# Kernel tuning notes

Measured on AMD Instinct MI355X. Metric: run time of the kernel, lower is better.

## Reference

```python
import jax, jax.numpy as jnp
import numpy as np

N_NODES, N_EDGES, N_GRAPHS = 30000, 70000, 1024
TOWERS, F_IN, F_OUT, N_LAYERS = 5, 75, 15, 4
DEG_HIST = np.array([0.0, 100.0, 400.0, 300.0, 50.0], dtype=np.float32)
AVG_DEG_LOG = float((np.log(np.arange(len(DEG_HIST)) + 1.0) * DEG_HIST).sum() / DEG_HIST.sum())


def setup_inputs():
    key = jax.random.key(0)
    ks = jax.random.split(key, 16)
    g = lambda k, shp, fan: jax.random.normal(k, shp, jnp.float32) * (1.0 / np.sqrt(fan))
    return dict(
        x=jax.random.randint(ks[0], (N_NODES,), 0, 21),
        edge_index=jax.random.randint(ks[1], (2, N_EDGES), 0, N_NODES),
        edge_attr=jax.random.randint(ks[2], (N_EDGES,), 0, 4),
        batch=jnp.sort(jax.random.randint(ks[3], (N_NODES,), 0, N_GRAPHS)),
        node_emb=g(ks[4], (21, 75), 75),
        edge_emb=g(ks[5], (4, 50), 50),
        enc_w=g(ks[6], (N_LAYERS, 50, 75), 50),
        enc_b=jnp.zeros((N_LAYERS, 75), jnp.float32),
        pre_w=g(ks[7], (N_LAYERS, TOWERS, 3 * F_IN, F_IN), 3 * F_IN),
        pre_b=jnp.zeros((N_LAYERS, TOWERS, F_IN), jnp.float32),
        post_w=g(ks[8], (N_LAYERS, TOWERS, 13 * F_IN, F_OUT), 13 * F_IN),
        post_b=jnp.zeros((N_LAYERS, TOWERS, F_OUT), jnp.float32),
        lin_w=g(ks[9], (N_LAYERS, 75, 75), 75),
        lin_b=jnp.zeros((N_LAYERS, 75), jnp.float32),
        bn_g=jnp.ones((N_LAYERS, 75), jnp.float32),
        bn_b=jnp.zeros((N_LAYERS, 75), jnp.float32),
        mlp_w1=g(ks[10], (75, 50), 75), mlp_b1=jnp.zeros((50,), jnp.float32),
        mlp_w2=g(ks[11], (50, 25), 50), mlp_b2=jnp.zeros((25,), jnp.float32),
        mlp_w3=g(ks[12], (25, 1), 25), mlp_b3=jnp.zeros((1,), jnp.float32),
    )


def _pna_layer(h, src, dst, e_enc, pw, pb, qw, qb, lw, lb):
    n = h.shape[0]
    # message: cat[x_i, x_j, edge_enc] shared across towers, per-tower pre-NN
    msg = jnp.concatenate([h[dst], h[src], e_enc], axis=-1)            # [E, 3*F_in]
    m = jnp.einsum('ef,tfo->eto', msg, pw) + pb                        # [E, T, F_in]
    deg = jax.ops.segment_sum(jnp.ones((m.shape[0],), m.dtype), dst, n)
    has = (deg > 0)[:, None, None]
    cnt = jnp.maximum(deg, 1.0)[:, None, None]                         # clamp(1)
    mean = jax.ops.segment_sum(m, dst, n) / cnt
    mean_sq = jax.ops.segment_sum(m * m, dst, n) / cnt
    std = jnp.sqrt(jax.nn.relu(mean_sq - mean * mean) + 1e-5)
    mn = jnp.where(has, jax.ops.segment_min(m, dst, n), 0.0)
    mx = jnp.where(has, jax.ops.segment_max(m, dst, n), 0.0)
    agg = jnp.concatenate([mean, mn, mx, std], axis=-1)                # [N, T, 4*F_in]
    amp = jnp.log(cnt + 1.0) / AVG_DEG_LOG                             # amplification scaler
    scaled = jnp.concatenate([agg, agg * amp, agg / amp], axis=-1)     # [N, T, 12*F_in]
    post_in = jnp.concatenate(
        [jnp.broadcast_to(h[:, None, :], (n, TOWERS, F_IN)), scaled], axis=-1)  # [N, T, 13*F_in]
    out = jnp.einsum('ntf,tfo->nto', post_in, qw) + qb                 # [N, T, F_out]
    return out.reshape(n, TOWERS * F_OUT) @ lw + lb                    # [N, 75]


def _bn_relu(h, g, b):
    mu = h.mean(axis=0)
    var = h.var(axis=0)
    return jax.nn.relu((h - mu) * jax.lax.rsqrt(var + 1e-5) * g + b)


def reference(x, edge_index, edge_attr, batch, node_emb, edge_emb, enc_w, enc_b,
              pre_w, pre_b, post_w, post_b, lin_w, lin_b, bn_g, bn_b,
              mlp_w1, mlp_b1, mlp_w2, mlp_b2, mlp_w3, mlp_b3):
    h = node_emb[x]                      # [N, 75]
    e = edge_emb[edge_attr]              # [E, 50]
    src, dst = edge_index[0], edge_index[1]
    for l in range(N_LAYERS):
        e_enc = e @ enc_w[l] + enc_b[l]  # [E, 75]
        h = _bn_relu(_pna_layer(h, src, dst, e_enc, pre_w[l], pre_b[l],
                                post_w[l], post_b[l], lin_w[l], lin_b[l]),
                     bn_g[l], bn_b[l])
    hg = jax.ops.segment_sum(h, batch, N_GRAPHS)   # global_add_pool -> [G, 75]
    z = jax.nn.relu(hg @ mlp_w1 + mlp_b1)
    z = jax.nn.relu(z @ mlp_w2 + mlp_b2)
    return z @ mlp_w3 + mlp_b3
```

## Files before the change

### kernel.cpp

```cpp
#include <hip/hip_runtime.h>
#include <hip/hip_bf16.h>
#include <float.h>
#include <math.h>

#define NN 30000
#define NE 70000
#define NG 1024
#define NT 5
#define FI 75
#define NL 4

#define AMP_DENOM 1.1824939264481302f

#define ABW 832
#define AGW 1600
#define HBW 96
#define ZW 76

typedef __attribute__((ext_vector_type(8))) short bf16x8;
typedef __attribute__((ext_vector_type(4))) float f32x4;

__device__ __forceinline__ float bf2f(unsigned short u) {
    return __uint_as_float(((unsigned int)u) << 16);
}
__device__ __forceinline__ unsigned short f2bf(float f) {
    __hip_bfloat16 h = __float2bfloat16(f);
    return *reinterpret_cast<unsigned short*>(&h);
}

__global__ __launch_bounds__(256) void k_deg(const int* __restrict__ dst, int* __restrict__ deg) {
    int e = blockIdx.x * 256 + threadIdx.x;
    if (e < NE) atomicAdd(&deg[dst[e]], 1);
}

__global__ __launch_bounds__(1024) void k_scan(const int* __restrict__ deg, int* __restrict__ rowptr) {
    __shared__ int wsum[16];
    __shared__ int s_carry;
    int tid = threadIdx.x;
    int lane = tid & 63, wv = tid >> 6;
    if (tid == 0) s_carry = 0;
    __syncthreads();
    for (int base = 0; base < NN; base += 1024) {
        int i = base + tid;
        int v = (i < NN) ? deg[i] : 0;
        int x = v;
        #pragma unroll
        for (int off = 1; off < 64; off <<= 1) {
            int t = __shfl_up(x, off);
            if (lane >= off) x += t;
        }
        if (lane == 63) wsum[wv] = x;
        __syncthreads();
        if (tid < 16) {
            int y = wsum[tid];
            #pragma unroll
            for (int off = 1; off < 16; off <<= 1) {
                int t = __shfl_up(y, off);
                if (tid >= off) y += t;
            }
            wsum[tid] = y;
        }
        __syncthreads();
        int wbase = ((wv > 0) ? wsum[wv - 1] : 0) + s_carry;
        if (i < NN) rowptr[i] = wbase + x - v;
        int tot = wsum[15];
        __syncthreads();
        if (tid == 0) s_carry += tot;
    }
    __syncthreads();
    if (tid == 0) rowptr[NN] = s_carry;
}

__global__ __launch_bounds__(256) void k_scatter(const int* __restrict__ src, const int* __restrict__ dst,
                                                 const int* __restrict__ attr, const int* __restrict__ rowptr,
                                                 int* __restrict__ fill, int* __restrict__ csr) {
    int e = blockIdx.x * 256 + threadIdx.x;
    if (e < NE) {
        int d = dst[e];
        int pos = rowptr[d] + atomicAdd(&fill[d], 1);
        csr[pos] = src[e] | (attr[e] << 20);
    }
}

__global__ __launch_bounds__(256) void k_amp(const int* __restrict__ rowptr,
                                             float* __restrict__ amp, float* __restrict__ inv) {
    int n = blockIdx.x * 256 + threadIdx.x;
    if (n < NN) {
        int dg = rowptr[n + 1] - rowptr[n];
        float cnt = fmaxf((float)dg, 1.0f);
        float a = logf(cnt + 1.0f) * (1.0f / AMP_DENOM);
        amp[n] = a;
        inv[n] = 1.0f / a;
    }
}

__global__ __launch_bounds__(256) void k_h0(const int* __restrict__ x, const float* __restrict__ emb,
                                            unsigned short* __restrict__ hb) {
    int idx = blockIdx.x * 256 + threadIdx.x;
    if (idx < NN * HBW) {
        int n = idx / HBW, f = idx % HBW;
        hb[idx] = (f < FI) ? f2bf(emb[x[n] * FI + f]) : (unsigned short)0;
    }
}

__global__ __launch_bounds__(256) void k_wprep5(const float* __restrict__ post_w,
                                                unsigned short* __restrict__ Wp5) {
    int idx = blockIdx.x * 256 + threadIdx.x;
    if (idx >= NL * NT * 3 * 10 * 512) return;
    int e = idx & 7;
    int lane = (idx >> 3) & 63;
    int ks = (idx >> 9) % 10;
    int s = (idx / 5120) % 3;
    int t = (idx / 15360) % NT;
    int l = idx / 76800;
    int lr = lane & 15, lq = lane >> 4;
    int kk = ks * 32 + lq * 8 + e;
    float val = 0.0f;
    if (kk < 304 && lr < 15) {
        int stat = kk / 76, of = kk - stat * 76;
        if (of < 75)
            val = post_w[((size_t)(l * NT + t) * 975 + 75 + s * 300 + stat * 75 + of) * 15 + lr];
    }
    Wp5[idx] = f2bf(val);
}

__global__ __launch_bounds__(256) void k_wprep2f(const float* __restrict__ pre_w,
                                                 const float* __restrict__ post_w,
                                                 unsigned short* __restrict__ Wp2f) {
    int idx = blockIdx.x * 256 + threadIdx.x;
    if (idx >= NL * 52 * 3 * 512) return;
    int e = idx & 7;
    int lane = (idx >> 3) & 63;
    int ks = (idx >> 9) % 3;
    int nt = (idx / 1536) % 52;
    int l = idx / (1536 * 52);
    int lr = lane & 15, lq = lane >> 4;
    int j = nt * 16 + lr;
    int k = ks * 32 + lq * 8 + e;
    float val = 0.0f;
    if (k < 75 && j < 825) {
        if (j < 375) {
            int t = j / 75, o = j % 75;
            val = pre_w[((size_t)(l * NT + t) * 225 + k) * FI + o];
        } else if (j < 750) {
            int jm = j - 375;
            int t = jm / 75, o = jm % 75;
            val = pre_w[((size_t)(l * NT + t) * 225 + 75 + k) * FI + o];
        } else {
            int c = j - 750;
            int t = c / 15, o = c % 15;
            val = post_w[((size_t)(l * NT + t) * 975 + k) * 15 + o];
        }
    }
    Wp2f[idx] = f2bf(val);
}

__global__ __launch_bounds__(256) void k_wprep4(const float* __restrict__ lin_w,
                                                unsigned short* __restrict__ linTp) {
    int idx = blockIdx.x * 256 + threadIdx.x;
    if (idx >= NL * 5 * 3 * 512) return;
    int e = idx & 7;
    int lane = (idx >> 3) & 63;
    int ks = (idx >> 9) % 3;
    int nt = (idx / 1536) % 5;
    int l = idx / 7680;
    int lr = lane & 15, lq = lane >> 4;
    int c = nt * 16 + lr;
    int k = ks * 32 + lq * 8 + e;
    float v = 0.0f;
    if (k < 75 && c < 75) v = lin_w[(size_t)l * 5625 + k * 75 + c];
    linTp[idx] = f2bf(v);
}

__global__ __launch_bounds__(384) void k_tbl4(const float* __restrict__ edge_emb, const float* __restrict__ enc_w,
                                              const float* __restrict__ enc_b, const float* __restrict__ pre_w,
                                              const float* __restrict__ pre_b, float* __restrict__ tbl4) {
    __shared__ float e4[4][FI];
    int l = blockIdx.x;
    int tid = threadIdx.x;
    float* tbl = tbl4 + l * 1500;
    if (tid < 300) {
        int a = tid / FI, f = tid % FI;
        float acc = enc_b[l * FI + f];
        for (int k = 0; k < 50; k++)
            acc += edge_emb[a * 50 + k] * enc_w[(l * 50 + k) * FI + f];
        e4[a][f] = acc;
    }
    __syncthreads();
    for (int idx = tid; idx < 4 * 375; idx += 384) {
        int a = idx / 375, c = idx % 375;
        int t = c / FI, o = c % FI;
        const float* wp = pre_w + ((size_t)(l * NT + t) * 225 + 150) * FI + o;
        float acc = pre_b[(l * NT + t) * FI + o];
        for (int f = 0; f < FI; f++)
            acc += e4[a][f] * wp[f * FI];
        tbl[idx] = acc;
    }
}

__global__ __launch_bounds__(256) void k_bnh(const float* __restrict__ z, const float* __restrict__ bnsum,
                                             const float* __restrict__ bng, const float* __restrict__ bnb,
                                             unsigned short* __restrict__ hb) {
    __shared__ float s_sc[75], s_sh[75];
    int tid = threadIdx.x;
    if (tid < 75) {
        float mu = bnsum[tid] * (1.0f / NN);
        float msq = bnsum[76 + tid] * (1.0f / NN);
        float var = msq - mu * mu;
        float sc = rsqrtf(var + 1e-5f) * bng[tid];
        s_sc[tid] = sc;
        s_sh[tid] = bnb[tid] - mu * sc;
    }
    __syncthreads();
    int idx = blockIdx.x * 256 + tid;
    if (idx < NN * HBW) {
        int n = idx / HBW, c = idx % HBW;
        float v = 0.0f;
        if (c < 75) v = fmaxf(z[(size_t)n * ZW + c] * s_sc[c] + s_sh[c], 0.0f);
        hb[idx] = (c < 75) ? f2bf(v) : (unsigned short)0;
    }
}

__global__ __launch_bounds__(256) void k_preab(const unsigned short* __restrict__ hb,
                                               const unsigned short* __restrict__ Wp2f,
                                               int l, __hip_bfloat16* __restrict__ ABH) {
    __shared__ __align__(16) unsigned short sA[128 * 104];
    int tid = threadIdx.x;
    int m0 = blockIdx.x * 128;
    int jt0 = blockIdx.y * 13;

    const uint4* hsrc = (const uint4*)hb;
    for (int c = tid; c < 128 * 12; c += 256) {
        int r = c / 12, q = c % 12;
        int n = m0 + r;
        uint4 v = make_uint4(0, 0, 0, 0);
        if (n < NN) v = hsrc[(size_t)n * 12 + q];
        *(uint4*)&sA[r * 104 + q * 8] = v;
    }
    __syncthreads();

    int w = tid >> 6, lane = tid & 63;
    int mw = w * 32;
    int lr = lane & 15, lq = lane >> 4;

    bf16x8 af[2][3];
    #pragma unroll
    for (int mt = 0; mt < 2; mt++)
        #pragma unroll
        for (int ks = 0; ks < 3; ks++)
            af[mt][ks] = *(const bf16x8*)&sA[(mw + mt * 16 + lr) * 104 + ks * 32 + lq * 8];

    f32x4 acc[13][2];
    #pragma unroll
    for (int nt = 0; nt < 13; nt++)
        #pragma unroll
        for (int mt = 0; mt < 2; mt++)
            acc[nt][mt] = (f32x4){0.0f, 0.0f, 0.0f, 0.0f};

    const unsigned short* wp = Wp2f + ((size_t)l * 52 + jt0) * 3 * 512;
    #pragma unroll
    for (int nt = 0; nt < 13; nt++) {
        #pragma unroll
        for (int ks = 0; ks < 3; ks++) {
            bf16x8 bf = *(const bf16x8*)&wp[(nt * 3 + ks) * 512 + lane * 8];
            acc[nt][0] = __builtin_amdgcn_mfma_f32_16x16x32_bf16(bf, af[0][ks], acc[nt][0], 0, 0, 0);
            acc[nt][1] = __builtin_amdgcn_mfma_f32_16x16x32_bf16(bf, af[1][ks], acc[nt][1], 0, 0, 0);
        }
    }

    unsigned short* abo = (unsigned short*)ABH;
    int j0 = jt0 * 16;
    #pragma unroll
    for (int mt = 0; mt < 2; mt++) {
        int n = m0 + mw + mt * 16 + lr;
        if (n < NN) {
            #pragma unroll
            for (int nt = 0; nt < 13; nt++) {
                int c0 = j0 + nt * 16 + lq * 4;
                ushort4 us;
                us.x = f2bf(acc[nt][mt][0]);
                us.y = f2bf(acc[nt][mt][1]);
                us.z = f2bf(acc[nt][mt][2]);
                us.w = f2bf(acc[nt][mt][3]);
                *(ushort4*)&abo[(size_t)n * ABW + c0] = us;
            }
        }
    }
}

__global__ __launch_bounds__(256) void k_gather(const __hip_bfloat16* __restrict__ ABH,
                                                const float* __restrict__ tbl,
                                                const int* __restrict__ rowptr, const int* __restrict__ csr,
                                                unsigned short* __restrict__ AGG) {
    __shared__ float s_tbl[1500];
    int tid = threadIdx.x;
    for (int i = tid; i < 1500; i += 256) s_tbl[i] = tbl[i];
    __syncthreads();

    int w = tid >> 6, l = tid & 63;
    int n = blockIdx.x * 4 + w;
    int base = rowptr[n];
    int dg = rowptr[n + 1] - base;

    float sum[6], ss[6], mn[6], mx[6];
    #pragma unroll
    for (int j = 0; j < 6; j++) { sum[j] = 0.f; ss[j] = 0.f; mn[j] = FLT_MAX; mx[j] = -FLT_MAX; }

    const unsigned short* abu = (const unsigned short*)ABH;
    int k = 0;
    for (; k + 1 < dg; k += 2) {
        int pk0 = csr[base + k], pk1 = csr[base + k + 1];
        const unsigned short* bp0 = abu + (size_t)(pk0 & 0xFFFFF) * ABW + 375;
        const unsigned short* bp1 = abu + (size_t)(pk1 & 0xFFFFF) * ABW + 375;
        const float* tp0 = s_tbl + (pk0 >> 20) * 375;
        const float* tp1 = s_tbl + (pk1 >> 20) * 375;
        #pragma unroll
        for (int j = 0; j < 6; j++) {
            int f = l + 64 * j;
            if (f < 375) {
                float v0 = bf2f(bp0[f]) + tp0[f];
                float v1 = bf2f(bp1[f]) + tp1[f];
                sum[j] += v0 + v1;
                ss[j] += v0 * v0 + v1 * v1;
                mn[j] = fminf(mn[j], fminf(v0, v1));
                mx[j] = fmaxf(mx[j], fmaxf(v0, v1));
            }
        }
    }
    if (k < dg) {
        int pk0 = csr[base + k];
        const unsigned short* bp0 = abu + (size_t)(pk0 & 0xFFFFF) * ABW + 375;
        const float* tp0 = s_tbl + (pk0 >> 20) * 375;
        #pragma unroll
        for (int j = 0; j < 6; j++) {
            int f = l + 64 * j;
            if (f < 375) {
                float v0 = bf2f(bp0[f]) + tp0[f];
                sum[j] += v0; ss[j] += v0 * v0;
                mn[j] = fminf(mn[j], v0); mx[j] = fmaxf(mx[j], v0);
            }
        }
    }

    unsigned short* out = AGG + (size_t)n * AGW;
    if (dg > 0) {
        float rc = 1.0f / (float)dg;
        const unsigned short* ap = abu + (size_t)n * ABW;
        #pragma unroll
        for (int j = 0; j < 6; j++) {
            int f = l + 64 * j;
            if (f < 375) {
                int t = f / 75, of = f - t * 75;
                int o = t * 320 + of;
                float Af = bf2f(ap[f]);
                float mean = sum[j] * rc;
                float var = ss[j] * rc - mean * mean;
                out[o]       = f2bf(Af + mean);
                out[o + 76]  = f2bf(Af + mn[j]);
                out[o + 152] = f2bf(Af + mx[j]);
                out[o + 228] = f2bf(sqrtf(fmaxf(var, 0.0f) + 1e-5f));
            }
        }
    } else {
        unsigned short zz = 0;
        unsigned short sd = f2bf(0.0031622776601683794f);
        #pragma unroll
        for (int j = 0; j < 6; j++) {
            int f = l + 64 * j;
            if (f < 375) {
                int t = f / 75, of = f - t * 75;
                int o = t * 320 + of;
                out[o] = zz; out[o + 76] = zz; out[o + 152] = zz; out[o + 228] = sd;
            }
        }
    }
    for (int i = l; i < 80; i += 64) out[(i >> 4) * 320 + 304 + (i & 15)] = 0;
    if (l < 20) out[(l >> 2) * 320 + (l & 3) * 76 + 75] = 0;
}

__global__ __launch_bounds__(256) void k_post(const __hip_bfloat16* __restrict__ ABH,
                                              const unsigned short* __restrict__ AGG,
                                              const unsigned short* __restrict__ Wp5,
                                              const unsigned short* __restrict__ linTp,
                                              const float* __restrict__ amp_a, const float* __restrict__ inv_a,
                                              const float* __restrict__ post_b, const float* __restrict__ lin_b,
                                              int l, float* __restrict__ z, float* __restrict__ bnsum) {
    __shared__ __align__(16) unsigned short s_y[64 * 104];
    __shared__ float s_bn[152];

    int tid = threadIdx.x;
    int n0 = blockIdx.x * 64;
    int w = tid >> 6, lane = tid & 63;
    int lr = lane & 15, lq = lane >> 4;

    if (tid < 152) s_bn[tid] = 0.0f;
    for (int i = tid; i < 64 * 29; i += 256) {
        int r = i / 29, c = 75 + i % 29;
        s_y[r * 104 + c] = 0;
    }

    const unsigned short* abu = (const unsigned short*)ABH;
    int mynode = n0 + w * 16 + lr;
    int mclamp = (mynode < NN) ? mynode : (NN - 1);
    float amp = amp_a[mclamp], inv = inv_a[mclamp];

    for (int t = 0; t < NT; t++) {
        const unsigned short* wp = Wp5 + (size_t)(l * NT + t) * 3 * 10 * 512;
        const unsigned short* ap = AGG + (size_t)mclamp * AGW + t * 320;

        f32x4 ac0 = {0, 0, 0, 0}, ac1 = {0, 0, 0, 0}, ac2 = {0, 0, 0, 0};
        #pragma unroll
        for (int ks = 0; ks < 10; ks++) {
            bf16x8 a = *(const bf16x8*)&ap[ks * 32 + lq * 8];
            bf16x8 b0 = *(const bf16x8*)&wp[(0 * 10 + ks) * 512 + lane * 8];
            bf16x8 b1 = *(const bf16x8*)&wp[(1 * 10 + ks) * 512 + lane * 8];
            bf16x8 b2 = *(const bf16x8*)&wp[(2 * 10 + ks) * 512 + lane * 8];
            ac0 = __builtin_amdgcn_mfma_f32_16x16x32_bf16(b0, a, ac0, 0, 0, 0);
            ac1 = __builtin_amdgcn_mfma_f32_16x16x32_bf16(b1, a, ac1, 0, 0, 0);
            ac2 = __builtin_amdgcn_mfma_f32_16x16x32_bf16(b2, a, ac2, 0, 0, 0);
        }
        #pragma unroll
        for (int r = 0; r < 4; r++) {
            int f = lq * 4 + r;
            if (f < 15) {
                float qb = post_b[(l * NT + t) * 15 + f];
                float ht = bf2f(abu[(size_t)mclamp * ABW + 750 + t * 15 + f]);
                float y = ac0[r] + amp * ac1[r] + inv * ac2[r] + ht + qb;
                s_y[(w * 16 + lr) * 104 + t * 15 + f] = f2bf(y);
            }
        }
    }
    __syncthreads();

    const unsigned short* lp = linTp + (size_t)l * 5 * 3 * 512;
    bf16x8 ya[3];
    #pragma unroll
    for (int ks = 0; ks < 3; ks++)
        ya[ks] = *(const bf16x8*)&s_y[(w * 16 + lr) * 104 + ks * 32 + lq * 8];

    #pragma unroll
    for (int nt = 0; nt < 5; nt++) {
        f32x4 a2 = {0, 0, 0, 0};
        #pragma unroll
        for (int ks = 0; ks < 3; ks++) {
            bf16x8 bb = *(const bf16x8*)&lp[(nt * 3 + ks) * 512 + lane * 8];
            a2 = __builtin_amdgcn_mfma_f32_16x16x32_bf16(bb, ya[ks], a2, 0, 0, 0);
        }
        int c0 = nt * 16 + lq * 4;
        float v[4], vm[4], vm2[4];
        #pragma unroll
        for (int r = 0; r < 4; r++) {
            int c = c0 + r;
            v[r] = (c < 75) ? (a2[r] + lin_b[l * 75 + c]) : 0.0f;
            bool ok = (c < 75) && (mynode < NN);
            vm[r] = ok ? v[r] : 0.0f;
            vm2[r] = ok ? v[r] * v[r] : 0.0f;
        }
        if (mynode < NN) {
            if (c0 + 3 < 75) {
                float4 st = make_float4(v[0], v[1], v[2], v[3]);
                *(float4*)&z[(size_t)mynode * ZW + c0] = st;
            } else {
                #pragma unroll
                for (int r = 0; r < 4; r++)
                    if (c0 + r < 75) z[(size_t)mynode * ZW + c0 + r] = v[r];
            }
        }
        #pragma unroll
        for (int r = 0; r < 4; r++) {
            #pragma unroll
            for (int off = 1; off < 16; off <<= 1) {
                vm[r] += __shfl_xor(vm[r], off);
                vm2[r] += __shfl_xor(vm2[r], off);
            }
        }
        if (lr == 0) {
            #pragma unroll
            for (int r = 0; r < 4; r++) {
                int c = c0 + r;
                if (c < 75) {
                    atomicAdd(&s_bn[c], vm[r]);
                    atomicAdd(&s_bn[76 + c], vm2[r]);
                }
            }
        }
    }
    __syncthreads();
    if (tid < 75) {
        atomicAdd(&bnsum[tid], s_bn[tid]);
        atomicAdd(&bnsum[76 + tid], s_bn[76 + tid]);
    }
}

__global__ __launch_bounds__(256) void k_pool(const float* __restrict__ z, const float* __restrict__ bnsum3,
                                              const float* __restrict__ bng, const float* __restrict__ bnb,
                                              const int* __restrict__ batch, float* __restrict__ hg) {
    __shared__ float s_sc[75], s_sh[75];
    int tid = threadIdx.x;
    if (tid < 75) {
        float mu = bnsum3[tid] * (1.0f / NN);
        float msq = bnsum3[76 + tid] * (1.0f / NN);
        float var = msq - mu * mu;
        float sc = rsqrtf(var + 1e-5f) * bng[tid];
        s_sc[tid] = sc;
        s_sh[tid] = bnb[tid] - mu * sc;
    }
    __syncthreads();
    int idx = blockIdx.x * 256 + tid;
    if (idx < NN * 75) {
        int n = idx / 75, f = idx % 75;
        float v = fmaxf(z[(size_t)n * ZW + f] * s_sc[f] + s_sh[f], 0.0f);
        atomicAdd(&hg[batch[n] * 75 + f], v);
    }
}

__global__ __launch_bounds__(64) void k_mlp(const float* __restrict__ hg,
                                            const float* __restrict__ w1, const float* __restrict__ b1,
                                            const float* __restrict__ w2, const float* __restrict__ b2,
                                            const float* __restrict__ w3, const float* __restrict__ b3,
                                            float* __restrict__ out) {
    __shared__ float zin[75], z1[50], z2[25];
    int g = blockIdx.x, tid = threadIdx.x;
    for (int k = tid; k < 75; k += 64) zin[k] = hg[g * 75 + k];
    __syncthreads();
    if (tid < 50) {
        float acc = b1[tid];
        for (int k = 0; k < 75; k++) acc += zin[k] * w1[k * 50 + tid];
        z1[tid] = fmaxf(acc, 0.0f);
    }
    __syncthreads();
    if (tid < 25) {
        float acc = b2[tid];
        for (int k = 0; k < 50; k++) acc += z1[k] * w2[k * 25 + tid];
        z2[tid] = fmaxf(acc, 0.0f);
    }
    __syncthreads();
    if (tid == 0) {
        float acc = b3[0];
        for (int k = 0; k < 25; k++) acc += z2[k] * w3[k];
        out[g] = acc;
    }
}

extern "C" void kernel_launch(void* const* d_in, const int* in_sizes, int n_in,
                              void* d_out, int out_size, void* d_ws, size_t ws_size,
                              hipStream_t stream) {
    const int* x        = (const int*)d_in[0];
    const int* ei       = (const int*)d_in[1];
    const int* eattr    = (const int*)d_in[2];
    const int* batch    = (const int*)d_in[3];
    const float* node_emb = (const float*)d_in[4];
    const float* edge_emb = (const float*)d_in[5];
    const float* enc_w  = (const float*)d_in[6];
    const float* enc_b  = (const float*)d_in[7];
    const float* pre_w  = (const float*)d_in[8];
    const float* pre_b  = (const float*)d_in[9];
    const float* post_w = (const float*)d_in[10];
    const float* post_b = (const float*)d_in[11];
    const float* lin_w  = (const float*)d_in[12];
    const float* lin_b  = (const float*)d_in[13];
    const float* bn_g   = (const float*)d_in[14];
    const float* bn_b   = (const float*)d_in[15];
    const float* w1     = (const float*)d_in[16];
    const float* b1     = (const float*)d_in[17];
    const float* w2     = (const float*)d_in[18];
    const float* b2     = (const float*)d_in[19];
    const float* w3     = (const float*)d_in[20];
    const float* b3     = (const float*)d_in[21];

    char* p = (char*)d_ws;
    auto carve = [&](size_t bytes) -> char* {
        char* r = p;
        p += ((bytes + 255) & ~(size_t)255);
        return r;
    };
    __hip_bfloat16* ABH = (__hip_bfloat16*)carve((size_t)NN * ABW * 2);
    unsigned short* AGG = (unsigned short*)carve((size_t)NN * AGW * 2);
    float* z     = (float*)carve((size_t)NN * ZW * 4);
    unsigned short* hb = (unsigned short*)carve((size_t)NN * HBW * 2);
    unsigned short* Wp2f  = (unsigned short*)carve((size_t)NL * 52 * 3 * 512 * 2);
    unsigned short* Wp5   = (unsigned short*)carve((size_t)NL * NT * 3 * 10 * 512 * 2);
    unsigned short* linTp = (unsigned short*)carve((size_t)NL * 5 * 3 * 512 * 2);
    float* tbl4  = (float*)carve((size_t)NL * 1500 * 4);
    int* deg     = (int*)carve(NN * 4);
    int* rowptr  = (int*)carve((NN + 1) * 4);
    int* fill    = (int*)carve(NN * 4);
    int* csr     = (int*)carve(NE * 4);
    float* bnsum = (float*)carve((size_t)NL * 152 * 4);
    float* amp_a = (float*)carve(NN * 4);
    float* inv_a = (float*)carve(NN * 4);
    float* hg    = (float*)carve((size_t)NG * 75 * 4);

    hipMemsetAsync(deg, 0, NN * 4, stream);
    hipMemsetAsync(fill, 0, NN * 4, stream);
    hipMemsetAsync(hg, 0, (size_t)NG * 75 * 4, stream);
    hipMemsetAsync(bnsum, 0, (size_t)NL * 152 * 4, stream);

    k_deg<<<(NE + 255) / 256, 256, 0, stream>>>(ei + NE, deg);
    k_scan<<<1, 1024, 0, stream>>>(deg, rowptr);
    k_scatter<<<(NE + 255) / 256, 256, 0, stream>>>(ei, ei + NE, eattr, rowptr, fill, csr);
    k_amp<<<(NN + 255) / 256, 256, 0, stream>>>(rowptr, amp_a, inv_a);
    k_h0<<<(NN * HBW + 255) / 256, 256, 0, stream>>>(x, node_emb, hb);
    k_wprep5<<<(NL * NT * 3 * 10 * 512 + 255) / 256, 256, 0, stream>>>(post_w, Wp5);
    k_wprep2f<<<(NL * 52 * 3 * 512 + 255) / 256, 256, 0, stream>>>(pre_w, post_w, Wp2f);
    k_wprep4<<<(NL * 5 * 3 * 512 + 255) / 256, 256, 0, stream>>>(lin_w, linTp);
    k_tbl4<<<NL, 384, 0, stream>>>(edge_emb, enc_w, enc_b, pre_w, pre_b, tbl4);

    for (int l = 0; l < NL; l++) {
        if (l > 0)
            k_bnh<<<(NN * HBW + 255) / 256, 256, 0, stream>>>(
                z, bnsum + (l - 1) * 152, bn_g + (l - 1) * 75, bn_b + (l - 1) * 75, hb);
        k_preab<<<dim3((NN + 127) / 128, 4), 256, 0, stream>>>(hb, Wp2f, l, ABH);
        k_gather<<<NN / 4, 256, 0, stream>>>(ABH, tbl4 + l * 1500, rowptr, csr, AGG);
        k_post<<<(NN + 63) / 64, 256, 0, stream>>>(ABH, AGG, Wp5, linTp, amp_a, inv_a,
                                                   post_b, lin_b, l, z, bnsum + l * 152);
    }

    k_pool<<<(NN * 75 + 255) / 256, 256, 0, stream>>>(z, bnsum + 3 * 152, bn_g + 3 * 75, bn_b + 3 * 75,
                                                      batch, hg);
    k_mlp<<<NG, 64, 0, stream>>>(hg, w1, b1, w2, b2, w3, b3, (float*)d_out);
}
```

Before: 590.4 us.

## Fuse neighbor aggregation and post-tower MLP into one kernel via shared memory

Merges the gather/aggregate kernel and the post-NN kernel into a single kernel that handles 16 nodes per block with 5 waves. Aggregated features stay in LDS instead of taking a round trip through a global AGG buffer, and each wave computes one tower and one output tile. This drops the 96 MB-scale AGG write and read plus one launch per layer. In exchange the gather parallelism per block is lower (5 waves share 16 nodes), LDS use per block is larger, and the block count rises, which may hurt occupancy and multiply the BN partial-sum atomics.

After: 787.0 us. +33.3%, slower.

```diff
diff --git a/kernel.cpp b/kernel.cpp
--- a/kernel.cpp
+++ b/kernel.cpp
@@ -13,9 +13,9 @@
 #define AMP_DENOM 1.1824939264481302f
 
 #define ABW 832
-#define AGW 1600
 #define HBW 96
 #define ZW 76
+#define AGS 1608
 
 typedef __attribute__((ext_vector_type(8))) short bf16x8;
 typedef __attribute__((ext_vector_type(4))) float f32x4;
@@ -288,130 +288,127 @@
     }
 }
 
-__global__ __launch_bounds__(256) void k_gather(const __hip_bfloat16* __restrict__ ABH,
-                                                const float* __restrict__ tbl,
-                                                const int* __restrict__ rowptr, const int* __restrict__ csr,
-                                                unsigned short* __restrict__ AGG) {
+__global__ __launch_bounds__(320) void k_gp(const __hip_bfloat16* __restrict__ ABH,
+                                            const float* __restrict__ tbl,
+                                            const int* __restrict__ rowptr, const int* __restrict__ csr,
+                                            const unsigned short* __restrict__ Wp5,
+                                            const unsigned short* __restrict__ linTp,
+                                            const float* __restrict__ amp_a, const float* __restrict__ inv_a,
+                                            const float* __restrict__ post_b, const float* __restrict__ lin_b,
+                                            int l, float* __restrict__ z, float* __restrict__ bnsum) {
+    __shared__ __align__(16) unsigned short s_agg[16 * AGS];
+    __shared__ __align__(16) unsigned short s_y[16 * 104];
     __shared__ float s_tbl[1500];
+    __shared__ float s_bn[152];
+
     int tid = threadIdx.x;
-    for (int i = tid; i < 1500; i += 256) s_tbl[i] = tbl[i];
-    __syncthreads();
-
-    int w = tid >> 6, l = tid & 63;
-    int n = blockIdx.x * 4 + w;
-    int base = rowptr[n];
-    int dg = rowptr[n + 1] - base;
-
-    float sum[6], ss[6], mn[6], mx[6];
-    #pragma unroll
-    for (int j = 0; j < 6; j++) { sum[j] = 0.f; ss[j] = 0.f; mn[j] = FLT_MAX; mx[j] = -FLT_MAX; }
-
-    const unsigned short* abu = (const unsigned short*)ABH;
-    int k = 0;
-    for (; k + 1 < dg; k += 2) {
-        int pk0 = csr[base + k], pk1 = csr[base + k + 1];
-        const unsigned short* bp0 = abu + (size_t)(pk0 & 0xFFFFF) * ABW + 375;
-        const unsigned short* bp1 = abu + (size_t)(pk1 & 0xFFFFF) * ABW + 375;
-        const float* tp0 = s_tbl + (pk0 >> 20) * 375;
-        const float* tp1 = s_tbl + (pk1 >> 20) * 375;
-        #pragma unroll
-        for (int j = 0; j < 6; j++) {
-            int f = l + 64 * j;
-            if (f < 375) {
-                float v0 = bf2f(bp0[f]) + tp0[f];
-                float v1 = bf2f(bp1[f]) + tp1[f];
-                sum[j] += v0 + v1;
-                ss[j] += v0 * v0 + v1 * v1;
-                mn[j] = fminf(mn[j], fminf(v0, v1));
-                mx[j] = fmaxf(mx[j], fmaxf(v0, v1));
-            }
-        }
-    }
-    if (k < dg) {
-        int pk0 = csr[base + k];
-        const unsigned short* bp0 = abu + (size_t)(pk0 & 0xFFFFF) * ABW + 375;
-        const float* tp0 = s_tbl + (pk0 >> 20) * 375;
-        #pragma unroll
-        for (int j = 0; j < 6; j++) {
-            int f = l + 64 * j;
-            if (f < 375) {
-                float v0 = bf2f(bp0[f]) + tp0[f];
-                sum[j] += v0; ss[j] += v0 * v0;
-                mn[j] = fminf(mn[j], v0); mx[j] = fmaxf(mx[j], v0);
-            }
-        }
-    }
-
-    unsigned short* out = AGG + (size_t)n * AGW;
-    if (dg > 0) {
-        float rc = 1.0f / (float)dg;
-        const unsigned short* ap = abu + (size_t)n * ABW;
-        #pragma unroll
-        for (int j = 0; j < 6; j++) {
-            int f = l + 64 * j;
-            if (f < 375) {
-                int t = f / 75, of = f - t * 75;
-                int o = t * 320 + of;
-                float Af = bf2f(ap[f]);
-                float mean = sum[j] * rc;
-                float var = ss[j] * rc - mean * mean;
-                out[o]       = f2bf(Af + mean);
-                out[o + 76]  = f2bf(Af + mn[j]);
-                out[o + 152] = f2bf(Af + mx[j]);
-                out[o + 228] = f2bf(sqrtf(fmaxf(var, 0.0f) + 1e-5f));
-            }
-        }
-    } else {
-        unsigned short zz = 0;
-        unsigned short sd = f2bf(0.0031622776601683794f);
-        #pragma unroll
-        for (int j = 0; j < 6; j++) {
-            int f = l + 64 * j;
-            if (f < 375) {
-                int t = f / 75, of = f - t * 75;
-                int o = t * 320 + of;
-                out[o] = zz; out[o + 76] = zz; out[o + 152] = zz; out[o + 228] = sd;
-            }
-        }
-    }
-    for (int i = l; i < 80; i += 64) out[(i >> 4) * 320 + 304 + (i & 15)] = 0;
-    if (l < 20) out[(l >> 2) * 320 + (l & 3) * 76 + 75] = 0;
-}
-
-__global__ __launch_bounds__(256) void k_post(const __hip_bfloat16* __restrict__ ABH,
-                                              const unsigned short* __restrict__ AGG,
-                                              const unsigned short* __restrict__ Wp5,
-                                              const unsigned short* __restrict__ linTp,
-                                              const float* __restrict__ amp_a, const float* __restrict__ inv_a,
-                                              const float* __restrict__ post_b, const float* __restrict__ lin_b,
-                                              int l, float* __restrict__ z, float* __restrict__ bnsum) {
-    __shared__ __align__(16) unsigned short s_y[64 * 104];
-    __shared__ float s_bn[152];
-
-    int tid = threadIdx.x;
-    int n0 = blockIdx.x * 64;
+    int n0 = blockIdx.x * 16;
     int w = tid >> 6, lane = tid & 63;
     int lr = lane & 15, lq = lane >> 4;
 
+    for (int i = tid; i < 1500; i += 320) s_tbl[i] = tbl[i];
     if (tid < 152) s_bn[tid] = 0.0f;
-    for (int i = tid; i < 64 * 29; i += 256) {
+    for (int i = tid; i < 16 * 100; i += 320) {
+        int node = i / 100, c = i % 100;
+        int pos = (c < 80) ? ((c >> 4) * 320 + 304 + (c & 15))
+                           : (((c - 80) >> 2) * 320 + ((c - 80) & 3) * 76 + 75);
+        s_agg[node * AGS + pos] = 0;
+    }
+    for (int i = tid; i < 16 * 29; i += 320) {
         int r = i / 29, c = 75 + i % 29;
         s_y[r * 104 + c] = 0;
     }
+    __syncthreads();
 
     const unsigned short* abu = (const unsigned short*)ABH;
-    int mynode = n0 + w * 16 + lr;
-    int mclamp = (mynode < NN) ? mynode : (NN - 1);
-    float amp = amp_a[mclamp], inv = inv_a[mclamp];
-
-    for (int t = 0; t < NT; t++) {
+
+    for (int ni = w; ni < 16; ni += 5) {
+        int node = n0 + ni;
+        int base = rowptr[node];
+        int dg = rowptr[node + 1] - base;
+
+        float sum[6], ss[6], mn[6], mx[6];
+        #pragma unroll
+        for (int j = 0; j < 6; j++) { sum[j] = 0.f; ss[j] = 0.f; mn[j] = FLT_MAX; mx[j] = -FLT_MAX; }
+
+        int k = 0;
+        for (; k + 1 < dg; k += 2) {
+            int pk0 = csr[base + k], pk1 = csr[base + k + 1];
+            const unsigned short* bp0 = abu + (size_t)(pk0 & 0xFFFFF) * ABW + 375;
+            const unsigned short* bp1 = abu + (size_t)(pk1 & 0xFFFFF) * ABW + 375;
+            const float* tp0 = s_tbl + (pk0 >> 20) * 375;
+            const float* tp1 = s_tbl + (pk1 >> 20) * 375;
+            #pragma unroll
+            for (int j = 0; j < 6; j++) {
+                int f = lane + 64 * j;
+                if (f < 375) {
+                    float v0 = bf2f(bp0[f]) + tp0[f];
+                    float v1 = bf2f(bp1[f]) + tp1[f];
+                    sum[j] += v0 + v1;
+                    ss[j] += v0 * v0 + v1 * v1;
+                    mn[j] = fminf(mn[j], fminf(v0, v1));
+                    mx[j] = fmaxf(mx[j], fmaxf(v0, v1));
+                }
+            }
+        }
+        if (k < dg) {
+            int pk0 = csr[base + k];
+            const unsigned short* bp0 = abu + (size_t)(pk0 & 0xFFFFF) * ABW + 375;
+            const float* tp0 = s_tbl + (pk0 >> 20) * 375;
+            #pragma unroll
+            for (int j = 0; j < 6; j++) {
+                int f = lane + 64 * j;
+                if (f < 375) {
+                    float v0 = bf2f(bp0[f]) + tp0[f];
+                    sum[j] += v0; ss[j] += v0 * v0;
+                    mn[j] = fminf(mn[j], v0); mx[j] = fmaxf(mx[j], v0);
+                }
+            }
+        }
+
+        unsigned short* out = &s_agg[ni * AGS];
+        if (dg > 0) {
+            float rc = 1.0f / (float)dg;
+            const unsigned short* ap = abu + (size_t)node * ABW;
+            #pragma unroll
+            for (int j = 0; j < 6; j++) {
+                int f = lane + 64 * j;
+                if (f < 375) {
+                    int t = f / 75, of = f - t * 75;
+                    int o = t * 320 + of;
+                    float Af = bf2f(ap[f]);
+                    float mean = sum[j] * rc;
+                    float var = ss[j] * rc - mean * mean;
+                    out[o]       = f2bf(Af + mean);
+                    out[o + 76]  = f2bf(Af + mn[j]);
+                    out[o + 152] = f2bf(Af + mx[j]);
+                    out[o + 228] = f2bf(sqrtf(fmaxf(var, 0.0f) + 1e-5f));
+                }
+            }
+        } else {
+            unsigned short sd = f2bf(0.0031622776601683794f);
+            #pragma unroll
+            for (int j = 0; j < 6; j++) {
+                int f = lane + 64 * j;
+                if (f < 375) {
+                    int t = f / 75, of = f - t * 75;
+                    int o = t * 320 + of;
+                    out[o] = 0; out[o + 76] = 0; out[o + 152] = 0; out[o + 228] = sd;
+                }
+            }
+        }
+    }
+    __syncthreads();
+
+    int mynode = n0 + lr;
+    float amp = amp_a[mynode], inv = inv_a[mynode];
+    {
+        int t = w;
         const unsigned short* wp = Wp5 + (size_t)(l * NT + t) * 3 * 10 * 512;
-        const unsigned short* ap = AGG + (size_t)mclamp * AGW + t * 320;
-
         f32x4 ac0 = {0, 0, 0, 0}, ac1 = {0, 0, 0, 0}, ac2 = {0, 0, 0, 0};
         #pragma unroll
         for (int ks = 0; ks < 10; ks++) {
-            bf16x8 a = *(const bf16x8*)&ap[ks * 32 + lq * 8];
+            bf16x8 a = *(const bf16x8*)&s_agg[lr * AGS + t * 320 + ks * 32 + lq * 8];
             bf16x8 b0 = *(const bf16x8*)&wp[(0 * 10 + ks) * 512 + lane * 8];
             bf16x8 b1 = *(const bf16x8*)&wp[(1 * 10 + ks) * 512 + lane * 8];
             bf16x8 b2 = *(const bf16x8*)&wp[(2 * 10 + ks) * 512 + lane * 8];
@@ -424,22 +421,22 @@
             int f = lq * 4 + r;
             if (f < 15) {
                 float qb = post_b[(l * NT + t) * 15 + f];
-                float ht = bf2f(abu[(size_t)mclamp * ABW + 750 + t * 15 + f]);
+                float ht = bf2f(abu[(size_t)mynode * ABW + 750 + t * 15 + f]);
                 float y = ac0[r] + amp * ac1[r] + inv * ac2[r] + ht + qb;
-                s_y[(w * 16 + lr) * 104 + t * 15 + f] = f2bf(y);
-            }
-        }
-    }
-    __syncthreads();
-
-    const unsigned short* lp = linTp + (size_t)l * 5 * 3 * 512;
-    bf16x8 ya[3];
-    #pragma unroll
-    for (int ks = 0; ks < 3; ks++)
-        ya[ks] = *(const bf16x8*)&s_y[(w * 16 + lr) * 104 + ks * 32 + lq * 8];
-
-    #pragma unroll
-    for (int nt = 0; nt < 5; nt++) {
+                s_y[lr * 104 + t * 15 + f] = f2bf(y);
+            }
+        }
+    }
+    __syncthreads();
+
+    {
+        const unsigned short* lp = linTp + (size_t)l * 5 * 3 * 512;
+        bf16x8 ya[3];
+        #pragma unroll
+        for (int ks = 0; ks < 3; ks++)
+            ya[ks] = *(const bf16x8*)&s_y[lr * 104 + ks * 32 + lq * 8];
+
+        int nt = w;
         f32x4 a2 = {0, 0, 0, 0};
         #pragma unroll
         for (int ks = 0; ks < 3; ks++) {
@@ -452,19 +449,16 @@
         for (int r = 0; r < 4; r++) {
             int c = c0 + r;
             v[r] = (c < 75) ? (a2[r] + lin_b[l * 75 + c]) : 0.0f;
-            bool ok = (c < 75) && (mynode < NN);
-            vm[r] = ok ? v[r] : 0.0f;
-            vm2[r] = ok ? v[r] * v[r] : 0.0f;
-        }
-        if (mynode < NN) {
-            if (c0 + 3 < 75) {
-                float4 st = make_float4(v[0], v[1], v[2], v[3]);
-                *(float4*)&z[(size_t)mynode * ZW + c0] = st;
-            } else {
-                #pragma unroll
-                for (int r = 0; r < 4; r++)
-                    if (c0 + r < 75) z[(size_t)mynode * ZW + c0 + r] = v[r];
-            }
+            vm[r] = (c < 75) ? v[r] : 0.0f;
+            vm2[r] = (c < 75) ? v[r] * v[r] : 0.0f;
+        }
+        if (c0 + 3 < 75) {
+            float4 st = make_float4(v[0], v[1], v[2], v[3]);
+            *(float4*)&z[(size_t)mynode * ZW + c0] = st;
+        } else {
+            #pragma unroll
+            for (int r = 0; r < 4; r++)
+                if (c0 + r < 75) z[(size_t)mynode * ZW + c0 + r] = v[r];
         }
         #pragma unroll
         for (int r = 0; r < 4; r++) {
@@ -575,7 +569,6 @@
         return r;
     };
     __hip_bfloat16* ABH = (__hip_bfloat16*)carve((size_t)NN * ABW * 2);
-    unsigned short* AGG = (unsigned short*)carve((size_t)NN * AGW * 2);
     float* z     = (float*)carve((size_t)NN * ZW * 4);
     unsigned short* hb = (unsigned short*)carve((size_t)NN * HBW * 2);
     unsigned short* Wp2f  = (unsigned short*)carve((size_t)NL * 52 * 3 * 512 * 2);
@@ -611,9 +604,8 @@
             k_bnh<<<(NN * HBW + 255) / 256, 256, 0, stream>>>(
                 z, bnsum + (l - 1) * 152, bn_g + (l - 1) * 75, bn_b + (l - 1) * 75, hb);
         k_preab<<<dim3((NN + 127) / 128, 4), 256, 0, stream>>>(hb, Wp2f, l, ABH);
-        k_gather<<<NN / 4, 256, 0, stream>>>(ABH, tbl4 + l * 1500, rowptr, csr, AGG);
-        k_post<<<(NN + 63) / 64, 256, 0, stream>>>(ABH, AGG, Wp5, linTp, amp_a, inv_a,
-                                                   post_b, lin_b, l, z, bnsum + l * 152);
+        k_gp<<<NN / 16, 320, 0, stream>>>(ABH, tbl4 + l * 1500, rowptr, csr, Wp5, linTp,
+                                          amp_a, inv_a, post_b, lin_b, l, z, bnsum + l * 152);
     }
 
     k_pool<<<(NN * 75 + 255) / 256, 256, 0, stream>>>(z, bnsum + 3 * 152, bn_g + 3 * 75, bn_b + 3 * 75,
```

## Split k_post work across towers per wave and vectorize BN-to-bf16 kernel

Applied to the files above, without the earlier changes.

k_post now processes 16 nodes per block with 5 waves, each wave handling one tower in the post-GEMM and one output tile in the linear GEMM, instead of each wave looping over all 5 towers for its own 16 nodes. This gives 5x more blocks and more parallel waves, meant to cut serial per-wave latency. k_bnh now has each thread produce 8 bf16 outputs from two float4 loads and write them with one 16-byte store, reducing thread count and memory transactions. The bounds checks are dropped because NN is divisible by 16. The cost is that every wave in a k_post block loads the same A rows, and there are more BN atomics per block.

Measured after the change: 727.5 us. 23.2% more time.

```diff
diff --git a/kernel.cpp b/kernel.cpp
--- a/kernel.cpp
+++ b/kernel.cpp
@@ -201,23 +201,46 @@
 __global__ __launch_bounds__(256) void k_bnh(const float* __restrict__ z, const float* __restrict__ bnsum,
                                              const float* __restrict__ bng, const float* __restrict__ bnb,
                                              unsigned short* __restrict__ hb) {
-    __shared__ float s_sc[75], s_sh[75];
+    __shared__ float s_sc[76], s_sh[76];
     int tid = threadIdx.x;
-    if (tid < 75) {
-        float mu = bnsum[tid] * (1.0f / NN);
-        float msq = bnsum[76 + tid] * (1.0f / NN);
-        float var = msq - mu * mu;
-        float sc = rsqrtf(var + 1e-5f) * bng[tid];
-        s_sc[tid] = sc;
-        s_sh[tid] = bnb[tid] - mu * sc;
+    if (tid < 76) {
+        if (tid < 75) {
+            float mu = bnsum[tid] * (1.0f / NN);
+            float msq = bnsum[76 + tid] * (1.0f / NN);
+            float var = msq - mu * mu;
+            float sc = rsqrtf(var + 1e-5f) * bng[tid];
+            s_sc[tid] = sc;
+            s_sh[tid] = bnb[tid] - mu * sc;
+        } else {
+            s_sc[tid] = 0.0f;
+            s_sh[tid] = 0.0f;
+        }
     }
     __syncthreads();
     int idx = blockIdx.x * 256 + tid;
-    if (idx < NN * HBW) {
-        int n = idx / HBW, c = idx % HBW;
-        float v = 0.0f;
-        if (c < 75) v = fmaxf(z[(size_t)n * ZW + c] * s_sc[c] + s_sh[c], 0.0f);
-        hb[idx] = (c < 75) ? f2bf(v) : (unsigned short)0;
+    if (idx < NN * 12) {
+        int n = idx / 12, q = idx % 12;
+        int c0 = q * 8;
+        unsigned short r[8];
+        if (c0 < 72) {
+            float4 a = *(const float4*)&z[(size_t)n * ZW + c0];
+            float4 b = *(const float4*)&z[(size_t)n * ZW + c0 + 4];
+            float vv[8] = {a.x, a.y, a.z, a.w, b.x, b.y, b.z, b.w};
+            #pragma unroll
+            for (int j = 0; j < 8; j++)
+                r[j] = f2bf(fmaxf(vv[j] * s_sc[c0 + j] + s_sh[c0 + j], 0.0f));
+        } else if (c0 == 72) {
+            float4 a = *(const float4*)&z[(size_t)n * ZW + 72];
+            float vv[4] = {a.x, a.y, a.z, a.w};
+            #pragma unroll
+            for (int j = 0; j < 8; j++)
+                r[j] = (j < 3) ? f2bf(fmaxf(vv[j] * s_sc[72 + j] + s_sh[72 + j], 0.0f))
+                               : (unsigned short)0;
+        } else {
+            #pragma unroll
+            for (int j = 0; j < 8; j++) r[j] = 0;
+        }
+        *(uint4*)&hb[(size_t)n * HBW + c0] = *(uint4*)r;
     }
 }
 
@@ -378,35 +401,35 @@
     if (l < 20) out[(l >> 2) * 320 + (l & 3) * 76 + 75] = 0;
 }
 
-__global__ __launch_bounds__(256) void k_post(const __hip_bfloat16* __restrict__ ABH,
+__global__ __launch_bounds__(320) void k_post(const __hip_bfloat16* __restrict__ ABH,
                                               const unsigned short* __restrict__ AGG,
                                               const unsigned short* __restrict__ Wp5,
                                               const unsigned short* __restrict__ linTp,
                                               const float* __restrict__ amp_a, const float* __restrict__ inv_a,
                                               const float* __restrict__ post_b, const float* __restrict__ lin_b,
                                               int l, float* __restrict__ z, float* __restrict__ bnsum) {
-    __shared__ __align__(16) unsigned short s_y[64 * 104];
+    __shared__ __align__(16) unsigned short s_y[16 * 104];
     __shared__ float s_bn[152];
 
     int tid = threadIdx.x;
-    int n0 = blockIdx.x * 64;
+    int n0 = blockIdx.x * 16;
     int w = tid >> 6, lane = tid & 63;
     int lr = lane & 15, lq = lane >> 4;
 
     if (tid < 152) s_bn[tid] = 0.0f;
-    for (int i = tid; i < 64 * 29; i += 256) {
+    for (int i = tid; i < 16 * 29; i += 320) {
         int r = i / 29, c = 75 + i % 29;
         s_y[r * 104 + c] = 0;
     }
 
     const unsigned short* abu = (const unsigned short*)ABH;
-    int mynode = n0 + w * 16 + lr;
-    int mclamp = (mynode < NN) ? mynode : (NN - 1);
-    float amp = amp_a[mclamp], inv = inv_a[mclamp];
-
-    for (int t = 0; t < NT; t++) {
+    int mynode = n0 + lr;
+    float amp = amp_a[mynode], inv = inv_a[mynode];
+
+    {
+        int t = w;
         const unsigned short* wp = Wp5 + (size_t)(l * NT + t) * 3 * 10 * 512;
-        const unsigned short* ap = AGG + (size_t)mclamp * AGW + t * 320;
+        const unsigned short* ap = AGG + (size_t)mynode * AGW + t * 320;
 
         f32x4 ac0 = {0, 0, 0, 0}, ac1 = {0, 0, 0, 0}, ac2 = {0, 0, 0, 0};
         #pragma unroll
@@ -424,22 +447,22 @@
             int f = lq * 4 + r;
             if (f < 15) {
                 float qb = post_b[(l * NT + t) * 15 + f];
-                float ht = bf2f(abu[(size_t)mclamp * ABW + 750 + t * 15 + f]);
+                float ht = bf2f(abu[(size_t)mynode * ABW + 750 + t * 15 + f]);
                 float y = ac0[r] + amp * ac1[r] + inv * ac2[r] + ht + qb;
-                s_y[(w * 16 + lr) * 104 + t * 15 + f] = f2bf(y);
-            }
-        }
-    }
-    __syncthreads();
-
-    const unsigned short* lp = linTp + (size_t)l * 5 * 3 * 512;
-    bf16x8 ya[3];
-    #pragma unroll
-    for (int ks = 0; ks < 3; ks++)
-        ya[ks] = *(const bf16x8*)&s_y[(w * 16 + lr) * 104 + ks * 32 + lq * 8];
-
-    #pragma unroll
-    for (int nt = 0; nt < 5; nt++) {
+                s_y[lr * 104 + t * 15 + f] = f2bf(y);
+            }
+        }
+    }
+    __syncthreads();
+
+    {
+        const unsigned short* lp = linTp + (size_t)l * 5 * 3 * 512;
+        bf16x8 ya[3];
+        #pragma unroll
+        for (int ks = 0; ks < 3; ks++)
+            ya[ks] = *(const bf16x8*)&s_y[lr * 104 + ks * 32 + lq * 8];
+
+        int nt = w;
         f32x4 a2 = {0, 0, 0, 0};
         #pragma unroll
         for (int ks = 0; ks < 3; ks++) {
@@ -452,19 +475,16 @@
         for (int r = 0; r < 4; r++) {
             int c = c0 + r;
             v[r] = (c < 75) ? (a2[r] + lin_b[l * 75 + c]) : 0.0f;
-            bool ok = (c < 75) && (mynode < NN);
-            vm[r] = ok ? v[r] : 0.0f;
-            vm2[r] = ok ? v[r] * v[r] : 0.0f;
-        }
-        if (mynode < NN) {
-            if (c0 + 3 < 75) {
-                float4 st = make_float4(v[0], v[1], v[2], v[3]);
-                *(float4*)&z[(size_t)mynode * ZW + c0] = st;
-            } else {
-                #pragma unroll
-                for (int r = 0; r < 4; r++)
-                    if (c0 + r < 75) z[(size_t)mynode * ZW + c0 + r] = v[r];
-            }
+            vm[r] = (c < 75) ? v[r] : 0.0f;
+            vm2[r] = (c < 75) ? v[r] * v[r] : 0.0f;
+        }
+        if (c0 + 3 < 75) {
+            float4 st = make_float4(v[0], v[1], v[2], v[3]);
+            *(float4*)&z[(size_t)mynode * ZW + c0] = st;
+        } else {
+            #pragma unroll
+            for (int r = 0; r < 4; r++)
+                if (c0 + r < 75) z[(size_t)mynode * ZW + c0 + r] = v[r];
         }
         #pragma unroll
         for (int r = 0; r < 4; r++) {
@@ -608,12 +628,12 @@
 
     for (int l = 0; l < NL; l++) {
         if (l > 0)
-            k_bnh<<<(NN * HBW + 255) / 256, 256, 0, stream>>>(
+            k_bnh<<<(NN * 12 + 255) / 256, 256, 0, stream>>>(
                 z, bnsum + (l - 1) * 152, bn_g + (l - 1) * 75, bn_b + (l - 1) * 75, hb);
         k_preab<<<dim3((NN + 127) / 128, 4), 256, 0, stream>>>(hb, Wp2f, l, ABH);
         k_gather<<<NN / 4, 256, 0, stream>>>(ABH, tbl4 + l * 1500, rowptr, csr, AGG);
-        k_post<<<(NN + 63) / 64, 256, 0, stream>>>(ABH, AGG, Wp5, linTp, amp_a, inv_a,
-                                                   post_b, lin_b, l, z, bnsum + l * 152);
+        k_post<<<NN / 16, 320, 0, stream>>>(ABH, AGG, Wp5, linTp, amp_a, inv_a,
+                                            post_b, lin_b, l, z, bnsum + l * 152);
     }
 
     k_pool<<<(NN * 75 + 255) / 256, 256, 0, stream>>>(z, bnsum + 3 * 152, bn_g + 3 * 75, bn_b + 3 * 75,
```
